# Kernel optimization log

Measured on AMD Instinct MI355X. Metric: run time of the kernel, lower is better.

Reference implementation:

```python
import jax, jax.numpy as jnp
import numpy as np

KS, STRIDE, DIL = 5, 1, 1
PAD = (KS + (KS - 1) * (DIL - 1) - 1) // 2
EPS = 1e-5


def _unfold_t(x):
    # x: (N, C, T, V) -> (N, C, T_out, KS, V), zero-padded temporal windows
    N, C, T, V = x.shape
    xp = jnp.pad(x, ((0, 0), (0, 0), (PAD, PAD), (0, 0)))
    t_out = (T + 2 * PAD - DIL * (KS - 1) - 1) // STRIDE + 1
    idx = jnp.arange(t_out)[:, None] * STRIDE + jnp.arange(KS)[None, :] * DIL  # (T_out, KS)
    return xp[:, :, idx, :]


def _bn2d(x, g, b):
    # training-mode BatchNorm2d: biased batch stats over (N, T, V)
    mu = jnp.mean(x, axis=(0, 2, 3), keepdims=True)
    var = jnp.var(x, axis=(0, 2, 3), keepdims=True)
    xn = (x - mu) * jax.lax.rsqrt(var + EPS)
    return xn * g[None, :, None, None] + b[None, :, None, None]


def setup_inputs() -> dict:
    key = jax.random.key(0)
    ks = jax.random.split(key, 8)
    N, C, T, V = 64, 64, 128, 25
    R, O = 8, 128
    s = 0.05
    return {
        "x": jax.random.normal(ks[0], (N, C, T, V), jnp.float32),
        "Wv": jax.random.normal(ks[1], (R, C), jnp.float32) * s,
        "bv": jax.random.normal(ks[2], (R,), jnp.float32) * s,
        "Ww": jax.random.normal(ks[3], (KS * KS, KS), jnp.float32) * s,
        "bw": jax.random.normal(ks[4], (KS * KS,), jnp.float32) * s,
        "g_bn": jnp.ones((R,), jnp.float32),
        "b_bn": jnp.zeros((R,), jnp.float32),
        "Wr": jax.random.normal(ks[5], (R, C), jnp.float32) * s,
        "br": jax.random.normal(ks[6], (R,), jnp.float32) * s,
        "g_r": jnp.ones((R,), jnp.float32),
        "b_r": jnp.zeros((R,), jnp.float32),
        "Wo": jax.random.normal(ks[7], (O, R), jnp.float32) * s,
        "bo": jnp.zeros((O,), jnp.float32),
        "g_o": jnp.ones((O,), jnp.float32),
        "b_o": jnp.zeros((O,), jnp.float32),
    }


def reference(x, Wv, bv, Ww, bw, g_bn, b_bn, Wr, br, g_r, b_r, Wo, bo, g_o, b_o):
    N, C, T, V = x.shape
    # convV (1x1) then unfold both x and v
    v0 = jnp.einsum('rc,nctv->nrtv', Wv, x) + bv[None, :, None, None]
    xu = _unfold_t(x)      # (N, C, T, W, V)
    vu = _unfold_t(v0)     # (N, R, T, W, V)
    # mean over channels, move window dim to channel position for convW
    m = jnp.mean(xu, axis=1).transpose(0, 2, 1, 3)  # (N, W, T, V)
    w = jnp.einsum('ow,nwtv->notv', Ww, m) + bw[None, :, None, None]
    weights = jnp.tanh(w.reshape(N, KS, KS, T, V))  # (N, W, W, T, V)
    att = jnp.einsum('nwutv,nctuv->nctv', weights, vu)  # (N, R, T, V)
    # residual 1x1 conv + BN (in_channels != out_channels -> conv path)
    res = _bn2d(jnp.einsum('rc,nctv->nrtv', Wr, x) + br[None, :, None, None], g_r, b_r)
    h = _bn2d(att, g_bn, b_bn) + res
    h = jnp.where(h >= 0, h, 0.1 * h)  # LeakyReLU(0.1)
    out = _bn2d(jnp.einsum('or,nrtv->notv', Wo, h) + bo[None, :, None, None], g_o, b_o)
    return out
```

## Files before the change

kernel.cpp:

```cpp
#include <hip/hip_runtime.h>
#include <math.h>

#define TV 3200
#define NTV 204800
#define NQ 51200
#define NB 400
constexpr float EPSF = 1e-5f;

typedef float f4 __attribute__((ext_vector_type(4)));

__device__ inline float fast_tanh(float x){
  float e = __expf(2.f*x);
  return 1.f - 2.f/(e + 1.f);
}

template<int NS>
__device__ inline void write_partials(float (&vals)[NS], float* __restrict__ out, float* lds){
  int lane = threadIdx.x & 63;
  int wid  = threadIdx.x >> 6;
  #pragma unroll
  for (int s = 0; s < NS; ++s){
    float v = vals[s];
    #pragma unroll
    for (int o = 32; o > 0; o >>= 1) v += __shfl_down(v, o);
    if (lane == 0) lds[s*2 + wid] = v;
  }
  __syncthreads();
  if ((int)threadIdx.x < NS){
    out[threadIdx.x*NB + blockIdx.x] = lds[threadIdx.x*2] + lds[threadIdx.x*2 + 1];
  }
}

__global__ __launch_bounds__(128) void k_proj(const float* __restrict__ x,
    const float* __restrict__ Wv, const float* __restrict__ bv,
    const float* __restrict__ Wr, const float* __restrict__ br,
    float* __restrict__ v0, float* __restrict__ r0, float* __restrict__ s,
    float* __restrict__ pr){
  __shared__ float lds[16*2];
  int tid = threadIdx.x;
  int p = blockIdx.x*128 + tid;
  int n = p / 800, q = p - n*800;
  int tv = q*4;
  const float* xp = x + (size_t)n*64*TV + tv;
  float av[8][4], ar[8][4];
  #pragma unroll
  for (int r = 0; r < 8; ++r)
    #pragma unroll
    for (int e = 0; e < 4; ++e){ av[r][e] = 0.f; ar[r][e] = 0.f; }
  float ss0 = 0.f, ss1 = 0.f, ss2 = 0.f, ss3 = 0.f;
  #pragma unroll 8
  for (int c = 0; c < 64; ++c){
    f4 xv = __builtin_nontemporal_load((const f4*)(xp + (size_t)c*TV));
    ss0 += xv.x; ss1 += xv.y; ss2 += xv.z; ss3 += xv.w;
    #pragma unroll
    for (int r = 0; r < 8; ++r){
      float wv = Wv[r*64 + c];
      float wr = Wr[r*64 + c];
      av[r][0] = fmaf(wv, xv.x, av[r][0]); av[r][1] = fmaf(wv, xv.y, av[r][1]);
      av[r][2] = fmaf(wv, xv.z, av[r][2]); av[r][3] = fmaf(wv, xv.w, av[r][3]);
      ar[r][0] = fmaf(wr, xv.x, ar[r][0]); ar[r][1] = fmaf(wr, xv.y, ar[r][1]);
      ar[r][2] = fmaf(wr, xv.z, ar[r][2]); ar[r][3] = fmaf(wr, xv.w, ar[r][3]);
    }
  }
  float4 sv; sv.x = ss0*0.015625f; sv.y = ss1*0.015625f; sv.z = ss2*0.015625f; sv.w = ss3*0.015625f;
  *(float4*)(s + (size_t)n*TV + tv) = sv;
  float* v0p = v0 + (size_t)n*8*TV + tv;
  float* r0p = r0 + (size_t)n*8*TV + tv;
  float vals[16];
  #pragma unroll
  for (int r = 0; r < 8; ++r){
    float bvr = bv[r], brr = br[r];
    float4 vv; vv.x = av[r][0]+bvr; vv.y = av[r][1]+bvr; vv.z = av[r][2]+bvr; vv.w = av[r][3]+bvr;
    *(float4*)(v0p + (size_t)r*TV) = vv;
    float r0e0 = ar[r][0]+brr, r0e1 = ar[r][1]+brr, r0e2 = ar[r][2]+brr, r0e3 = ar[r][3]+brr;
    float4 rv; rv.x = r0e0; rv.y = r0e1; rv.z = r0e2; rv.w = r0e3;
    *(float4*)(r0p + (size_t)r*TV) = rv;
    vals[r]   = r0e0 + r0e1 + r0e2 + r0e3;
    vals[8+r] = r0e0*r0e0 + r0e1*r0e1 + r0e2*r0e2 + r0e3*r0e3;
  }
  write_partials<16>(vals, pr, lds);
}

__global__ __launch_bounds__(128) void k_wat(const float* __restrict__ s,
    const float* __restrict__ Ww, const float* __restrict__ bw,
    const float* __restrict__ v0, float* __restrict__ att, float* __restrict__ patt){
  __shared__ float lds[16*2];
  int tid = threadIdx.x;
  int p = blockIdx.x*128 + tid;
  int n = p / 800, q = p - n*800;
  int tv = q*4;
  const float* sn  = s  + (size_t)n*TV;
  const float* v0n = v0 + (size_t)n*8*TV;
  float a[8][4];
  #pragma unroll
  for (int r = 0; r < 8; ++r)
    #pragma unroll
    for (int e = 0; e < 4; ++e) a[r][e] = 0.f;
  #pragma unroll
  for (int e = 0; e < 4; ++e){
    int tve = tv + e;
    int t = tve / 25;
    float m[5];
    #pragma unroll
    for (int k = 0; k < 5; ++k){
      int tt = t + k - 2;
      m[k] = (tt >= 0 && tt < 128) ? sn[tve + (k-2)*25] : 0.f;
    }
    float w2[5] = {0.f,0.f,0.f,0.f,0.f};
    #pragma unroll
    for (int w = 0; w < 5; ++w){
      #pragma unroll
      for (int u = 0; u < 5; ++u){
        int o = w*5 + u;
        float wo = bw[o];
        #pragma unroll
        for (int k = 0; k < 5; ++k) wo = fmaf(Ww[o*5+k], m[k], wo);
        w2[u] += fast_tanh(wo);
      }
    }
    #pragma unroll
    for (int u = 0; u < 5; ++u){
      int tt = t + u - 2;
      if (tt >= 0 && tt < 128){
        float wu = w2[u];
        const float* vp = v0n + tve + (u-2)*25;
        #pragma unroll
        for (int r = 0; r < 8; ++r) a[r][e] = fmaf(wu, vp[(size_t)r*TV], a[r][e]);
      }
    }
  }
  float* ap = att + (size_t)n*8*TV + tv;
  float vals[16];
  #pragma unroll
  for (int r = 0; r < 8; ++r){
    float4 av4; av4.x = a[r][0]; av4.y = a[r][1]; av4.z = a[r][2]; av4.w = a[r][3];
    *(float4*)(ap + (size_t)r*TV) = av4;
    vals[r]   = a[r][0] + a[r][1] + a[r][2] + a[r][3];
    vals[8+r] = a[r][0]*a[r][0] + a[r][1]*a[r][1] + a[r][2]*a[r][2] + a[r][3]*a[r][3];
  }
  write_partials<16>(vals, patt, lds);
}

__global__ __launch_bounds__(256) void k_bncoef(const float* __restrict__ pr,
    const float* __restrict__ patt,
    const float* __restrict__ g_bn, const float* __restrict__ b_bn,
    const float* __restrict__ g_r, const float* __restrict__ b_r,
    float* __restrict__ coef){
  __shared__ float lds[8];
  int b = blockIdx.x;
  bool isatt = (b >= 8);
  int r = isatt ? b - 8 : b;
  const float* ps = (isatt ? patt : pr) + r*NB;
  const float* pq = (isatt ? patt : pr) + (8+r)*NB;
  float s1 = 0.f, s2 = 0.f;
  for (int i = threadIdx.x; i < NB; i += 256){ s1 += ps[i]; s2 += pq[i]; }
  int lane = threadIdx.x & 63, wid = threadIdx.x >> 6;
  #pragma unroll
  for (int o = 32; o > 0; o >>= 1){ s1 += __shfl_down(s1, o); s2 += __shfl_down(s2, o); }
  if (lane == 0){ lds[wid] = s1; lds[4+wid] = s2; }
  __syncthreads();
  if (threadIdx.x == 0){
    float sum = lds[0]+lds[1]+lds[2]+lds[3];
    float sq  = lds[4]+lds[5]+lds[6]+lds[7];
    float mu  = sum / (float)NTV;
    float var = sq / (float)NTV - mu*mu;
    float g  = isatt ? g_bn[r] : g_r[r];
    float bb = isatt ? b_bn[r] : b_r[r];
    float a = g * rsqrtf(var + EPSF);
    float c = bb - a*mu;
    int base = isatt ? 0 : 16;
    coef[base + r] = a;
    coef[base + 8 + r] = c;
  }
}

__global__ __launch_bounds__(128) void k_h(const float* __restrict__ att,
    const float* __restrict__ r0, const float* __restrict__ coef,
    float* __restrict__ h, float* __restrict__ ph){
  __shared__ float lds[44*2];
  int tid = threadIdx.x;
  int p = blockIdx.x*128 + tid;
  int n = p / 800, q = p - n*800;
  int tv = q*4;
  const float* ap = att + (size_t)n*8*TV + tv;
  const float* rp = r0  + (size_t)n*8*TV + tv;
  float* hp = h + (size_t)n*8*TV + tv;
  float hv[8][4];
  #pragma unroll
  for (int r = 0; r < 8; ++r){
    float ca = coef[r], cc = coef[8+r], cr = coef[16+r], cd = coef[24+r];
    float4 av = *(const float4*)(ap + (size_t)r*TV);
    float4 rv = *(const float4*)(rp + (size_t)r*TV);
    float z0 = ca*av.x + cc + cr*rv.x + cd;
    float z1 = ca*av.y + cc + cr*rv.y + cd;
    float z2 = ca*av.z + cc + cr*rv.z + cd;
    float z3 = ca*av.w + cc + cr*rv.w + cd;
    hv[r][0] = (z0 >= 0.f) ? z0 : 0.1f*z0;
    hv[r][1] = (z1 >= 0.f) ? z1 : 0.1f*z1;
    hv[r][2] = (z2 >= 0.f) ? z2 : 0.1f*z2;
    hv[r][3] = (z3 >= 0.f) ? z3 : 0.1f*z3;
    float4 hh; hh.x = hv[r][0]; hh.y = hv[r][1]; hh.z = hv[r][2]; hh.w = hv[r][3];
    *(float4*)(hp + (size_t)r*TV) = hh;
  }
  float vals[44];
  #pragma unroll
  for (int r = 0; r < 8; ++r) vals[r] = hv[r][0] + hv[r][1] + hv[r][2] + hv[r][3];
  int cnt = 8;
  #pragma unroll
  for (int r = 0; r < 8; ++r){
    #pragma unroll
    for (int r2 = r; r2 < 8; ++r2){
      vals[cnt++] = hv[r][0]*hv[r2][0] + hv[r][1]*hv[r2][1]
                  + hv[r][2]*hv[r2][2] + hv[r][3]*hv[r2][3];
    }
  }
  write_partials<44>(vals, ph, lds);
}

__global__ __launch_bounds__(256) void k_hredfold(const float* __restrict__ ph,
    const float* __restrict__ Wo, const float* __restrict__ bo,
    const float* __restrict__ g_o, const float* __restrict__ b_o,
    float* __restrict__ fold, float* __restrict__ bfold){
  __shared__ float lds[44*4];
  __shared__ float hstat[44];
  __shared__ double muh[8];
  __shared__ double exx[8][8];
  int tid = threadIdx.x, lane = tid & 63, wid = tid >> 6;
  for (int j = 0; j < 44; ++j){
    float s1 = 0.f;
    for (int i = tid; i < NB; i += 256) s1 += ph[j*NB + i];
    #pragma unroll
    for (int o = 32; o > 0; o >>= 1) s1 += __shfl_down(s1, o);
    if (lane == 0) lds[j*4 + wid] = s1;
  }
  __syncthreads();
  if (tid < 44) hstat[tid] = lds[tid*4] + lds[tid*4+1] + lds[tid*4+2] + lds[tid*4+3];
  __syncthreads();
  if (tid < 8) muh[tid] = (double)hstat[tid] / (double)NTV;
  if (tid == 0){
    int cnt = 8;
    for (int r = 0; r < 8; ++r)
      for (int r2 = r; r2 < 8; ++r2){
        double e = (double)hstat[cnt++] / (double)NTV;
        exx[r][r2] = e; exx[r2][r] = e;
      }
  }
  __syncthreads();
  if (tid < 128){
    int o = tid;
    double w[8];
    for (int r = 0; r < 8; ++r) w[r] = (double)Wo[o*8+r];
    double bob = (double)bo[o];
    double mu = bob;
    for (int r = 0; r < 8; ++r) mu += w[r]*muh[r];
    double t = 0.0;
    for (int r = 0; r < 8; ++r)
      for (int r2 = 0; r2 < 8; ++r2) t += w[r]*w[r2]*exx[r][r2];
    double ey2 = t + 2.0*bob*(mu - bob) + bob*bob;
    double var = ey2 - mu*mu;
    double a = (double)g_o[o] / sqrt(var + (double)EPSF);
    for (int r = 0; r < 8; ++r) fold[o*8+r] = (float)(a * w[r]);
    bfold[o] = (float)(a * (bob - mu) + (double)b_o[o]);
  }
}

__global__ __launch_bounds__(128) void k_out(const float* __restrict__ h,
    const float* __restrict__ fold, const float* __restrict__ bfold,
    float* __restrict__ out){
  int tid = threadIdx.x;
  int p = blockIdx.x*128 + tid;
  int n = p / 800, q = p - n*800;
  int tv = q*4;
  const float* hp = h + (size_t)n*8*TV + tv;
  float hv[8][4];
  #pragma unroll
  for (int r = 0; r < 8; ++r){
    float4 v = *(const float4*)(hp + (size_t)r*TV);
    hv[r][0] = v.x; hv[r][1] = v.y; hv[r][2] = v.z; hv[r][3] = v.w;
  }
  float* op = out + (size_t)n*128*TV + tv;
  #pragma unroll 8
  for (int o = 0; o < 128; ++o){
    float b = bfold[o];
    float y0 = b, y1 = b, y2 = b, y3 = b;
    #pragma unroll
    for (int r = 0; r < 8; ++r){
      float w = fold[o*8+r];
      y0 = fmaf(w, hv[r][0], y0); y1 = fmaf(w, hv[r][1], y1);
      y2 = fmaf(w, hv[r][2], y2); y3 = fmaf(w, hv[r][3], y3);
    }
    f4 yy; yy.x = y0; yy.y = y1; yy.z = y2; yy.w = y3;
    __builtin_nontemporal_store(yy, (f4*)(op + (size_t)o*TV));
  }
}

extern "C" void kernel_launch(void* const* d_in, const int* in_sizes, int n_in,
                              void* d_out, int out_size, void* d_ws, size_t ws_size,
                              hipStream_t stream){
  const float* x    = (const float*)d_in[0];
  const float* Wv   = (const float*)d_in[1];
  const float* bv   = (const float*)d_in[2];
  const float* Ww   = (const float*)d_in[3];
  const float* bw   = (const float*)d_in[4];
  const float* g_bn = (const float*)d_in[5];
  const float* b_bn = (const float*)d_in[6];
  const float* Wr   = (const float*)d_in[7];
  const float* br   = (const float*)d_in[8];
  const float* g_r  = (const float*)d_in[9];
  const float* b_r  = (const float*)d_in[10];
  const float* Wo   = (const float*)d_in[11];
  const float* bo   = (const float*)d_in[12];
  const float* g_o  = (const float*)d_in[13];
  const float* b_o  = (const float*)d_in[14];

  float* ws = (float*)d_ws;
  size_t off = 0;
  float* v0   = ws + off; off += 1638400;
  float* r0   = ws + off; off += 1638400;
  float* s    = ws + off; off += 204800;
  float* att  = ws + off; off += 1638400;
  float* hbuf = ws + off; off += 1638400;
  float* pr   = ws + off; off += 16*NB;
  float* patt = ws + off; off += 16*NB;
  float* ph   = ws + off; off += 44*NB;
  float* coef = ws + off; off += 32;
  float* fold = ws + off; off += 1024;
  float* bfold= ws + off; off += 128;

  k_proj    <<<NB, 128, 0, stream>>>(x, Wv, bv, Wr, br, v0, r0, s, pr);
  k_wat     <<<NB, 128, 0, stream>>>(s, Ww, bw, v0, att, patt);
  k_bncoef  <<<16, 256, 0, stream>>>(pr, patt, g_bn, b_bn, g_r, b_r, coef);
  k_h       <<<NB, 128, 0, stream>>>(att, r0, coef, hbuf, ph);
  k_hredfold<<<1, 256, 0, stream>>>(ph, Wo, bo, g_o, b_o, fold, bfold);
  k_out     <<<NB, 128, 0, stream>>>(hbuf, fold, bfold, (float*)d_out);
}
```

Before: 257.6 us.

## Map one element per thread with 256-thread blocks and stage weights in LDS

Every elementwise kernel changes from four consecutive (t,v) elements per thread with float4 accesses to one element per thread. Blocks grow to 256 threads and the grid to 800 blocks, so four times as many threads are in flight to hide memory latency. The small weight and coefficient arrays (Wv/Wr, Ww/bw, BN coefficients, folded output weights) are first copied into shared memory. The cost is losing vectorized 128-bit loads and stores, a higher ratio of weight reads to FMAs, and twice as many partial-sum slots for the reduction kernels to read.

```diff
diff --git a/kernel.cpp b/kernel.cpp
--- a/kernel.cpp
+++ b/kernel.cpp
@@ -3,11 +3,8 @@
 
 #define TV 3200
 #define NTV 204800
-#define NQ 51200
-#define NB 400
+#define NB 800
 constexpr float EPSF = 1e-5f;
-
-typedef float f4 __attribute__((ext_vector_type(4)));
 
 __device__ inline float fast_tanh(float x){
   float e = __expf(2.f*x);
@@ -23,120 +20,102 @@
     float v = vals[s];
     #pragma unroll
     for (int o = 32; o > 0; o >>= 1) v += __shfl_down(v, o);
-    if (lane == 0) lds[s*2 + wid] = v;
+    if (lane == 0) lds[s*4 + wid] = v;
   }
   __syncthreads();
   if ((int)threadIdx.x < NS){
-    out[threadIdx.x*NB + blockIdx.x] = lds[threadIdx.x*2] + lds[threadIdx.x*2 + 1];
-  }
-}
-
-__global__ __launch_bounds__(128) void k_proj(const float* __restrict__ x,
+    out[threadIdx.x*NB + blockIdx.x] = lds[threadIdx.x*4+0] + lds[threadIdx.x*4+1]
+                                     + lds[threadIdx.x*4+2] + lds[threadIdx.x*4+3];
+  }
+}
+
+__global__ __launch_bounds__(256) void k_proj(const float* __restrict__ x,
     const float* __restrict__ Wv, const float* __restrict__ bv,
     const float* __restrict__ Wr, const float* __restrict__ br,
     float* __restrict__ v0, float* __restrict__ r0, float* __restrict__ s,
     float* __restrict__ pr){
-  __shared__ float lds[16*2];
-  int tid = threadIdx.x;
-  int p = blockIdx.x*128 + tid;
-  int n = p / 800, q = p - n*800;
-  int tv = q*4;
+  __shared__ float sWv[512], sWr[512], lds[16*4];
+  int tid = threadIdx.x;
+  for (int i = tid; i < 512; i += 256){ sWv[i] = Wv[i]; sWr[i] = Wr[i]; }
+  __syncthreads();
+  int p = blockIdx.x*256 + tid;
+  int n = p / TV, tv = p - n*TV;
   const float* xp = x + (size_t)n*64*TV + tv;
-  float av[8][4], ar[8][4];
-  #pragma unroll
-  for (int r = 0; r < 8; ++r)
-    #pragma unroll
-    for (int e = 0; e < 4; ++e){ av[r][e] = 0.f; ar[r][e] = 0.f; }
-  float ss0 = 0.f, ss1 = 0.f, ss2 = 0.f, ss3 = 0.f;
+  float av[8] = {0,0,0,0,0,0,0,0};
+  float ar[8] = {0,0,0,0,0,0,0,0};
+  float ssum = 0.f;
   #pragma unroll 8
   for (int c = 0; c < 64; ++c){
-    f4 xv = __builtin_nontemporal_load((const f4*)(xp + (size_t)c*TV));
-    ss0 += xv.x; ss1 += xv.y; ss2 += xv.z; ss3 += xv.w;
+    float xv = __builtin_nontemporal_load(xp + (size_t)c*TV);
+    ssum += xv;
     #pragma unroll
     for (int r = 0; r < 8; ++r){
-      float wv = Wv[r*64 + c];
-      float wr = Wr[r*64 + c];
-      av[r][0] = fmaf(wv, xv.x, av[r][0]); av[r][1] = fmaf(wv, xv.y, av[r][1]);
-      av[r][2] = fmaf(wv, xv.z, av[r][2]); av[r][3] = fmaf(wv, xv.w, av[r][3]);
-      ar[r][0] = fmaf(wr, xv.x, ar[r][0]); ar[r][1] = fmaf(wr, xv.y, ar[r][1]);
-      ar[r][2] = fmaf(wr, xv.z, ar[r][2]); ar[r][3] = fmaf(wr, xv.w, ar[r][3]);
+      av[r] = fmaf(sWv[r*64+c], xv, av[r]);
+      ar[r] = fmaf(sWr[r*64+c], xv, ar[r]);
     }
   }
-  float4 sv; sv.x = ss0*0.015625f; sv.y = ss1*0.015625f; sv.z = ss2*0.015625f; sv.w = ss3*0.015625f;
-  *(float4*)(s + (size_t)n*TV + tv) = sv;
+  s[p] = ssum * 0.015625f;
   float* v0p = v0 + (size_t)n*8*TV + tv;
   float* r0p = r0 + (size_t)n*8*TV + tv;
   float vals[16];
   #pragma unroll
   for (int r = 0; r < 8; ++r){
-    float bvr = bv[r], brr = br[r];
-    float4 vv; vv.x = av[r][0]+bvr; vv.y = av[r][1]+bvr; vv.z = av[r][2]+bvr; vv.w = av[r][3]+bvr;
-    *(float4*)(v0p + (size_t)r*TV) = vv;
-    float r0e0 = ar[r][0]+brr, r0e1 = ar[r][1]+brr, r0e2 = ar[r][2]+brr, r0e3 = ar[r][3]+brr;
-    float4 rv; rv.x = r0e0; rv.y = r0e1; rv.z = r0e2; rv.w = r0e3;
-    *(float4*)(r0p + (size_t)r*TV) = rv;
-    vals[r]   = r0e0 + r0e1 + r0e2 + r0e3;
-    vals[8+r] = r0e0*r0e0 + r0e1*r0e1 + r0e2*r0e2 + r0e3*r0e3;
+    v0p[(size_t)r*TV] = av[r] + bv[r];
+    float rr = ar[r] + br[r];
+    r0p[(size_t)r*TV] = rr;
+    vals[r] = rr; vals[8+r] = rr*rr;
   }
   write_partials<16>(vals, pr, lds);
 }
 
-__global__ __launch_bounds__(128) void k_wat(const float* __restrict__ s,
+__global__ __launch_bounds__(256) void k_wat(const float* __restrict__ s,
     const float* __restrict__ Ww, const float* __restrict__ bw,
     const float* __restrict__ v0, float* __restrict__ att, float* __restrict__ patt){
-  __shared__ float lds[16*2];
-  int tid = threadIdx.x;
-  int p = blockIdx.x*128 + tid;
-  int n = p / 800, q = p - n*800;
-  int tv = q*4;
-  const float* sn  = s  + (size_t)n*TV;
+  __shared__ float sWw[125], sbw[25], lds[16*4];
+  int tid = threadIdx.x;
+  if (tid < 125) sWw[tid] = Ww[tid];
+  if (tid < 25)  sbw[tid] = bw[tid];
+  __syncthreads();
+  int p = blockIdx.x*256 + tid;
+  int n = p / TV, tv = p - n*TV;
+  int t = tv / 25, v = tv - t*25;
+  const float* sn = s + (size_t)n*TV;
+  float m[5];
+  #pragma unroll
+  for (int k = 0; k < 5; ++k){
+    int tt = t + k - 2;
+    m[k] = (tt >= 0 && tt < 128) ? sn[tt*25 + v] : 0.f;
+  }
+  float w2[5] = {0.f,0.f,0.f,0.f,0.f};
+  #pragma unroll
+  for (int w = 0; w < 5; ++w){
+    #pragma unroll
+    for (int u = 0; u < 5; ++u){
+      int o = w*5 + u;
+      float wo = sbw[o];
+      #pragma unroll
+      for (int k = 0; k < 5; ++k) wo = fmaf(sWw[o*5+k], m[k], wo);
+      w2[u] += fast_tanh(wo);
+    }
+  }
   const float* v0n = v0 + (size_t)n*8*TV;
-  float a[8][4];
-  #pragma unroll
-  for (int r = 0; r < 8; ++r)
-    #pragma unroll
-    for (int e = 0; e < 4; ++e) a[r][e] = 0.f;
-  #pragma unroll
-  for (int e = 0; e < 4; ++e){
-    int tve = tv + e;
-    int t = tve / 25;
-    float m[5];
-    #pragma unroll
-    for (int k = 0; k < 5; ++k){
-      int tt = t + k - 2;
-      m[k] = (tt >= 0 && tt < 128) ? sn[tve + (k-2)*25] : 0.f;
-    }
-    float w2[5] = {0.f,0.f,0.f,0.f,0.f};
-    #pragma unroll
-    for (int w = 0; w < 5; ++w){
+  float a[8] = {0,0,0,0,0,0,0,0};
+  #pragma unroll
+  for (int u = 0; u < 5; ++u){
+    int tt = t + u - 2;
+    if (tt >= 0 && tt < 128){
+      float wu = w2[u];
+      const float* vp = v0n + tt*25 + v;
       #pragma unroll
-      for (int u = 0; u < 5; ++u){
-        int o = w*5 + u;
-        float wo = bw[o];
-        #pragma unroll
-        for (int k = 0; k < 5; ++k) wo = fmaf(Ww[o*5+k], m[k], wo);
-        w2[u] += fast_tanh(wo);
-      }
-    }
-    #pragma unroll
-    for (int u = 0; u < 5; ++u){
-      int tt = t + u - 2;
-      if (tt >= 0 && tt < 128){
-        float wu = w2[u];
-        const float* vp = v0n + tve + (u-2)*25;
-        #pragma unroll
-        for (int r = 0; r < 8; ++r) a[r][e] = fmaf(wu, vp[(size_t)r*TV], a[r][e]);
-      }
+      for (int r = 0; r < 8; ++r) a[r] = fmaf(wu, vp[(size_t)r*TV], a[r]);
     }
   }
   float* ap = att + (size_t)n*8*TV + tv;
   float vals[16];
   #pragma unroll
   for (int r = 0; r < 8; ++r){
-    float4 av4; av4.x = a[r][0]; av4.y = a[r][1]; av4.z = a[r][2]; av4.w = a[r][3];
-    *(float4*)(ap + (size_t)r*TV) = av4;
-    vals[r]   = a[r][0] + a[r][1] + a[r][2] + a[r][3];
-    vals[8+r] = a[r][0]*a[r][0] + a[r][1]*a[r][1] + a[r][2]*a[r][2] + a[r][3]*a[r][3];
+    ap[(size_t)r*TV] = a[r];
+    vals[r] = a[r]; vals[8+r] = a[r]*a[r];
   }
   write_partials<16>(vals, patt, lds);
 }
@@ -174,45 +153,34 @@
   }
 }
 
-__global__ __launch_bounds__(128) void k_h(const float* __restrict__ att,
+__global__ __launch_bounds__(256) void k_h(const float* __restrict__ att,
     const float* __restrict__ r0, const float* __restrict__ coef,
     float* __restrict__ h, float* __restrict__ ph){
-  __shared__ float lds[44*2];
-  int tid = threadIdx.x;
-  int p = blockIdx.x*128 + tid;
-  int n = p / 800, q = p - n*800;
-  int tv = q*4;
+  __shared__ float lds[44*4];
+  __shared__ float sc[32];
+  int tid = threadIdx.x;
+  if (tid < 32) sc[tid] = coef[tid];
+  __syncthreads();
+  int p = blockIdx.x*256 + tid;
+  int n = p / TV, tv = p - n*TV;
   const float* ap = att + (size_t)n*8*TV + tv;
   const float* rp = r0  + (size_t)n*8*TV + tv;
   float* hp = h + (size_t)n*8*TV + tv;
-  float hv[8][4];
-  #pragma unroll
-  for (int r = 0; r < 8; ++r){
-    float ca = coef[r], cc = coef[8+r], cr = coef[16+r], cd = coef[24+r];
-    float4 av = *(const float4*)(ap + (size_t)r*TV);
-    float4 rv = *(const float4*)(rp + (size_t)r*TV);
-    float z0 = ca*av.x + cc + cr*rv.x + cd;
-    float z1 = ca*av.y + cc + cr*rv.y + cd;
-    float z2 = ca*av.z + cc + cr*rv.z + cd;
-    float z3 = ca*av.w + cc + cr*rv.w + cd;
-    hv[r][0] = (z0 >= 0.f) ? z0 : 0.1f*z0;
-    hv[r][1] = (z1 >= 0.f) ? z1 : 0.1f*z1;
-    hv[r][2] = (z2 >= 0.f) ? z2 : 0.1f*z2;
-    hv[r][3] = (z3 >= 0.f) ? z3 : 0.1f*z3;
-    float4 hh; hh.x = hv[r][0]; hh.y = hv[r][1]; hh.z = hv[r][2]; hh.w = hv[r][3];
-    *(float4*)(hp + (size_t)r*TV) = hh;
+  float hv[8];
+  #pragma unroll
+  for (int r = 0; r < 8; ++r){
+    float z = sc[r]*ap[(size_t)r*TV] + sc[8+r] + sc[16+r]*rp[(size_t)r*TV] + sc[24+r];
+    hv[r] = (z >= 0.f) ? z : 0.1f*z;
+    hp[(size_t)r*TV] = hv[r];
   }
   float vals[44];
   #pragma unroll
-  for (int r = 0; r < 8; ++r) vals[r] = hv[r][0] + hv[r][1] + hv[r][2] + hv[r][3];
+  for (int r = 0; r < 8; ++r) vals[r] = hv[r];
   int cnt = 8;
   #pragma unroll
   for (int r = 0; r < 8; ++r){
     #pragma unroll
-    for (int r2 = r; r2 < 8; ++r2){
-      vals[cnt++] = hv[r][0]*hv[r2][0] + hv[r][1]*hv[r2][1]
-                  + hv[r][2]*hv[r2][2] + hv[r][3]*hv[r2][3];
-    }
+    for (int r2 = r; r2 < 8; ++r2) vals[cnt++] = hv[r]*hv[r2];
   }
   write_partials<44>(vals, ph, lds);
 }
@@ -264,33 +232,27 @@
   }
 }
 
-__global__ __launch_bounds__(128) void k_out(const float* __restrict__ h,
+__global__ __launch_bounds__(256) void k_out(const float* __restrict__ h,
     const float* __restrict__ fold, const float* __restrict__ bfold,
     float* __restrict__ out){
-  int tid = threadIdx.x;
-  int p = blockIdx.x*128 + tid;
-  int n = p / 800, q = p - n*800;
-  int tv = q*4;
+  __shared__ float sW[1024], sB[128];
+  int tid = threadIdx.x;
+  for (int i = tid; i < 1024; i += 256) sW[i] = fold[i];
+  if (tid < 128) sB[tid] = bfold[tid];
+  __syncthreads();
+  int p = blockIdx.x*256 + tid;
+  int n = p / TV, tv = p - n*TV;
   const float* hp = h + (size_t)n*8*TV + tv;
-  float hv[8][4];
-  #pragma unroll
-  for (int r = 0; r < 8; ++r){
-    float4 v = *(const float4*)(hp + (size_t)r*TV);
-    hv[r][0] = v.x; hv[r][1] = v.y; hv[r][2] = v.z; hv[r][3] = v.w;
-  }
+  float hv[8];
+  #pragma unroll
+  for (int r = 0; r < 8; ++r) hv[r] = hp[(size_t)r*TV];
   float* op = out + (size_t)n*128*TV + tv;
   #pragma unroll 8
   for (int o = 0; o < 128; ++o){
-    float b = bfold[o];
-    float y0 = b, y1 = b, y2 = b, y3 = b;
-    #pragma unroll
-    for (int r = 0; r < 8; ++r){
-      float w = fold[o*8+r];
-      y0 = fmaf(w, hv[r][0], y0); y1 = fmaf(w, hv[r][1], y1);
-      y2 = fmaf(w, hv[r][2], y2); y3 = fmaf(w, hv[r][3], y3);
-    }
-    f4 yy; yy.x = y0; yy.y = y1; yy.z = y2; yy.w = y3;
-    __builtin_nontemporal_store(yy, (f4*)(op + (size_t)o*TV));
+    float y = sB[o];
+    #pragma unroll
+    for (int r = 0; r < 8; ++r) y = fmaf(sW[o*8+r], hv[r], y);
+    __builtin_nontemporal_store(y, op + (size_t)o*TV);
   }
 }
 
@@ -327,10 +289,10 @@
   float* fold = ws + off; off += 1024;
   float* bfold= ws + off; off += 128;
 
-  k_proj    <<<NB, 128, 0, stream>>>(x, Wv, bv, Wr, br, v0, r0, s, pr);
-  k_wat     <<<NB, 128, 0, stream>>>(s, Ww, bw, v0, att, patt);
+  k_proj    <<<NB, 256, 0, stream>>>(x, Wv, bv, Wr, br, v0, r0, s, pr);
+  k_wat     <<<NB, 256, 0, stream>>>(s, Ww, bw, v0, att, patt);
   k_bncoef  <<<16, 256, 0, stream>>>(pr, patt, g_bn, b_bn, g_r, b_r, coef);
-  k_h       <<<NB, 128, 0, stream>>>(att, r0, coef, hbuf, ph);
+  k_h       <<<NB, 256, 0, stream>>>(att, r0, coef, hbuf, ph);
   k_hredfold<<<1, 256, 0, stream>>>(ph, Wo, bo, g_o, b_o, fold, bfold);
-  k_out     <<<NB, 128, 0, stream>>>(hbuf, fold, bfold, (float*)d_out);
-}
+  k_out     <<<NB, 256, 0, stream>>>(hbuf, fold, bfold, (float*)d_out);
+}
```

After: 282.9 us. +9.8%, slower.
